# Performance work log

Hardware: AMD Instinct MI355X
Metric: run time of the kernel (lower is better)

Reference implementation:

```python
import jax, jax.numpy as jnp
import numpy as np

SIM_THRESHOLD = 0.7  # suppression threshold on cosine similarity


def setup_inputs() -> dict:
    key = jax.random.key(0)
    k1, k2 = jax.random.split(key)
    tokens = jax.random.normal(k1, (4, 4096, 256), dtype=jnp.float32)
    scores = jax.random.uniform(k2, (4, 4096), dtype=jnp.float32)
    return {"tokens": tokens, "scores": scores}


def _nms_keep_sorted(sim_sorted):
    """Greedy NMS over tokens already sorted by descending score.

    sim_sorted: [N, N] pairwise cosine similarity in sorted order.
    Returns keep mask [N] (bool) in sorted order.
    """
    N = sim_sorted.shape[0]
    idx = jnp.arange(N)

    def step(suppressed, i):
        keep_i = jnp.logical_not(suppressed[i])
        row = sim_sorted[i]  # similarity of token i to all tokens
        # a kept token suppresses all later (lower-score) similar tokens
        suppressed = suppressed | (keep_i & (row > SIM_THRESHOLD) & (idx > i))
        return suppressed, keep_i

    _, keeps = jax.lax.scan(step, jnp.zeros(N, dtype=bool), idx)
    return keeps


def reference(tokens, scores):
    # tokens: [B, N, D], scores: [B, N]
    t = tokens / (jnp.linalg.norm(tokens, axis=-1, keepdims=True) + 1e-6)
    sim = jnp.einsum('bnd,bmd->bnm', t, t)  # [B, N, N] cosine similarity
    order = jnp.argsort(-scores, axis=-1)   # descending score order

    def per_batch(sim_b, order_b):
        sim_sorted = sim_b[order_b][:, order_b]          # reorder rows+cols
        keeps_sorted = _nms_keep_sorted(sim_sorted)      # [N] bool, sorted order
        keep = jnp.zeros_like(keeps_sorted).at[order_b].set(keeps_sorted)
        return keep

    keep = jax.vmap(per_batch)(sim, order)               # [B, N] bool
    masked_tokens = tokens * keep[..., None].astype(tokens.dtype)
    return masked_tokens, keep
```

## Files before the change

kernel.cpp:

```cpp
#include <hip/hip_runtime.h>

#define BATCH 4
#define N 4096
#define D 256
#define THR 0.7f
#define CAP 2048

typedef __attribute__((ext_vector_type(16))) float f32x16;

__device__ __forceinline__ unsigned int fflip(float f) {
    unsigned int u = __float_as_uint(f);
    return (u & 0x80000000u) ? ~u : (u | 0x80000000u);
}

__device__ __forceinline__ void gl_lds16(const unsigned char* g, unsigned char* l) {
    __builtin_amdgcn_global_load_lds(
        (const __attribute__((address_space(1))) unsigned int*)g,
        (__attribute__((address_space(3))) unsigned int*)l, 16, 0, 0);
}

__global__ __launch_bounds__(256) void norm_kernel(const float* __restrict__ tokens,
                                                   unsigned char* __restrict__ ts,
                                                   float* __restrict__ out,
                                                   float* __restrict__ keep_out,
                                                   int* __restrict__ cnt) {
    if (blockIdx.x == 0 && threadIdx.x < BATCH) cnt[threadIdx.x] = 0;
    int gw = (int)((blockIdx.x * 256 + threadIdx.x) >> 6);
    int lane = threadIdx.x & 63;
    const float4* p = (const float4*)(tokens + (size_t)gw * D);
    float4 v = p[lane];
    ((float4*)(out + (size_t)gw * D))[lane] = v;
    if (lane == 0) keep_out[gw] = 1.0f;
    float ss = v.x * v.x + v.y * v.y + v.z * v.z + v.w * v.w;
#pragma unroll
    for (int off = 32; off > 0; off >>= 1) ss += __shfl_xor(ss, off);
    float inv = 1.0f / (sqrtf(ss) + 1e-6f);
    unsigned int u = 0;
    u = __builtin_amdgcn_cvt_pk_fp8_f32(v.x * inv, v.y * inv, u, 0);
    u = __builtin_amdgcn_cvt_pk_fp8_f32(v.z * inv, v.w * inv, u, 1);
    *((unsigned int*)(ts + (size_t)gw * D + lane * 4)) = u;
}

__global__ __launch_bounds__(256, 5) void sim_kernel(const unsigned char* __restrict__ ts,
                                                     const float* __restrict__ scores,
                                                     unsigned long long* __restrict__ edges,
                                                     int* __restrict__ cnt) {
    __shared__ alignas(16) unsigned char smem[32768];
    int p = blockIdx.x;
    int b = blockIdx.y;
    int ti = (int)(32.5f - sqrtf(32.5f * 32.5f - 2.0f * (float)p));
    while (32 * ti - ti * (ti - 1) / 2 > p) --ti;
    while (32 * (ti + 1) - (ti + 1) * ti / 2 <= p) ++ti;
    int tj = ti + (p - (32 * ti - ti * (ti - 1) / 2));

    int t = threadIdx.x;
    int w = t >> 6;
    int L = t & 63;
    const unsigned char* base = ts + (size_t)b * N * D;

    int rl = L >> 3, sl = L & 7;
    const unsigned char* pa = base + (size_t)(ti * 128 + w * 8 + rl) * D + ((sl ^ rl) << 4);
    const unsigned char* pb = base + (size_t)(tj * 128 + w * 8 + rl) * D + ((sl ^ rl) << 4);
    unsigned char* la = smem + w * 1024;
    unsigned char* lb = smem + 16384 + w * 1024;

    int wr = w >> 1, wc = w & 1;
    int m = L & 31, h = L >> 5;
    int aA = (wr * 64 + m) * 128;
    int bB = 16384 + (wc * 64 + m) * 128;
    int swz = m & 7;
    int h8 = h * 8;

    f32x16 acc[2][2] = {};

#pragma unroll
    for (int s = 0; s < 2; ++s) {
#pragma unroll
        for (int i = 0; i < 4; ++i) {
            gl_lds16(pa + (size_t)i * 32 * D, la + i * 4096);
            gl_lds16(pb + (size_t)i * 32 * D, lb + i * 4096);
        }
        pa += 128; pb += 128;
        __syncthreads();
#pragma unroll
        for (int c = 0; c < 8; ++c) {
            int off = ((c ^ swz) << 4) + h8;
            long long a0 = *(const long long*)(smem + aA + off);
            long long a1 = *(const long long*)(smem + aA + 4096 + off);
            long long b0 = *(const long long*)(smem + bB + off);
            long long b1 = *(const long long*)(smem + bB + 4096 + off);
            acc[0][0] = __builtin_amdgcn_mfma_f32_32x32x16_fp8_fp8(a0, b0, acc[0][0], 0, 0, 0);
            acc[0][1] = __builtin_amdgcn_mfma_f32_32x32x16_fp8_fp8(a0, b1, acc[0][1], 0, 0, 0);
            acc[1][0] = __builtin_amdgcn_mfma_f32_32x32x16_fp8_fp8(a1, b0, acc[1][0], 0, 0, 0);
            acc[1][1] = __builtin_amdgcn_mfma_f32_32x32x16_fp8_fp8(a1, b1, acc[1][1], 0, 0, 0);
        }
        __syncthreads();
    }

    {
        float mx = -1e30f;
#pragma unroll
        for (int fa = 0; fa < 2; ++fa)
#pragma unroll
            for (int fb = 0; fb < 2; ++fb)
#pragma unroll
                for (int reg = 0; reg < 16; ++reg)
                    mx = fmaxf(mx, acc[fa][fb][reg]);
        if (!__any(mx > THR)) return;
    }

#pragma unroll
    for (int fa = 0; fa < 2; ++fa) {
#pragma unroll
        for (int fb = 0; fb < 2; ++fb) {
#pragma unroll
            for (int reg = 0; reg < 16; ++reg) {
                int row = (reg & 3) + 8 * (reg >> 2) + 4 * h;
                int ig = ti * 128 + wr * 64 + fa * 32 + row;
                int jg = tj * 128 + wc * 64 + fb * 32 + m;
                float v = acc[fa][fb][reg];
                if (jg > ig && v > THR) {
                    float si = scores[b * N + ig];
                    float sj = scores[b * N + jg];
                    int src, dst;
                    float ssrc;
                    if (si >= sj) { src = ig; dst = jg; ssrc = si; }
                    else          { src = jg; dst = ig; ssrc = sj; }
                    int pos = atomicAdd(&cnt[b], 1);
                    if (pos < CAP) {
                        unsigned long long kk =
                            ((unsigned long long)fflip(ssrc) << 24) |
                            ((unsigned long long)(unsigned int)(4095 - src) << 12) |
                            (unsigned long long)(unsigned int)dst;
                        edges[b * CAP + pos] = kk;
                    }
                }
            }
        }
    }
}

__global__ __launch_bounds__(256) void nms_kernel(const unsigned long long* __restrict__ edges,
                                                  const int* __restrict__ cnt,
                                                  float* __restrict__ keep_out,
                                                  float* __restrict__ out) {
    int b = blockIdx.x;
    __shared__ unsigned long long e[CAP];
    __shared__ unsigned int sup[N / 32];
    int n = cnt[b];
    if (n > CAP) n = CAP;
    if (n > 0) {
        for (int i = threadIdx.x; i < N / 32; i += 256) sup[i] = 0u;
        for (int i = threadIdx.x; i < CAP; i += 256)
            e[i] = (i < n) ? edges[b * CAP + i] : 0ull;
        __syncthreads();
        for (int k = 2; k <= CAP; k <<= 1) {
            for (int j = k >> 1; j > 0; j >>= 1) {
                for (int i = threadIdx.x; i < CAP; i += 256) {
                    int ixj = i ^ j;
                    if (ixj > i) {
                        unsigned long long a = e[i], cc = e[ixj];
                        bool up = ((i & k) == 0);
                        if (up ? (a < cc) : (a > cc)) { e[i] = cc; e[ixj] = a; }
                    }
                }
                __syncthreads();
            }
        }
        if (threadIdx.x == 0) {
            for (int tt = 0; tt < n; ++tt) {
                unsigned long long u = e[tt];
                int src = 4095 - (int)((u >> 12) & 0xFFFu);
                int dst = (int)(u & 0xFFFu);
                if (!((sup[src >> 5] >> (src & 31)) & 1u))
                    sup[dst >> 5] |= 1u << (dst & 31);
            }
        }
        __syncthreads();
        float4 z = make_float4(0.f, 0.f, 0.f, 0.f);
        for (int i = threadIdx.x; i < N; i += 256) {
            if ((sup[i >> 5] >> (i & 31)) & 1u) {
                keep_out[b * N + i] = 0.0f;
                float4* rowp = (float4*)(out + ((size_t)b * N + i) * D);
#pragma unroll
                for (int d = 0; d < D / 4; ++d) rowp[d] = z;
            }
        }
    }
}

extern "C" void kernel_launch(void* const* d_in, const int* in_sizes, int n_in,
                              void* d_out, int out_size, void* d_ws, size_t ws_size,
                              hipStream_t stream) {
    const float* tokens = (const float*)d_in[0];
    const float* scores = (const float*)d_in[1];

    char* ws = (char*)d_ws;
    int* cnt = (int*)ws;
    unsigned long long* edges = (unsigned long long*)(ws + 128);
    unsigned char* ts = (unsigned char*)(ws + 128 + BATCH * CAP * 8);

    float* out = (float*)d_out;
    float* keep_out = out + (size_t)BATCH * N * D;

    norm_kernel<<<(BATCH * N) / 4, 256, 0, stream>>>(tokens, ts, out, keep_out, cnt);
    dim3 g(528, BATCH);
    sim_kernel<<<g, 256, 0, stream>>>(ts, scores, edges, cnt);
    nms_kernel<<<BATCH, 256, 0, stream>>>(edges, cnt, keep_out, out);
}
```

Measured before the change: 91.92 us.

## Double-buffer sim kernel K loop in 64-byte chunks to overlap loads with MFMA

The sim kernel's K dimension is split into four 64-byte stages instead of two 128-byte stages. Two LDS buffers let the global-to-LDS loads for the next stage be issued before the MFMAs on the current stage. The LDS row stride and XOR swizzle are changed to match the 64-byte rows. The aim is to hide global-load latency behind compute, at the cost of more barriers and more loop iterations for a K dimension that is already short.

```diff
diff --git a/kernel.cpp b/kernel.cpp
--- a/kernel.cpp
+++ b/kernel.cpp
@@ -58,37 +58,47 @@
     int L = t & 63;
     const unsigned char* base = ts + (size_t)b * N * D;
 
-    int rl = L >> 3, sl = L & 7;
-    const unsigned char* pa = base + (size_t)(ti * 128 + w * 8 + rl) * D + ((sl ^ rl) << 4);
-    const unsigned char* pb = base + (size_t)(tj * 128 + w * 8 + rl) * D + ((sl ^ rl) << 4);
-    unsigned char* la = smem + w * 1024;
-    unsigned char* lb = smem + 16384 + w * 1024;
+    int rq = L >> 2;
+    int chunk = (L & 3) ^ ((L >> 3) & 3);
+    const unsigned char* pa = base + (size_t)(ti * 128 + w * 32 + rq) * D + (chunk << 4);
+    const unsigned char* pb = base + (size_t)(tj * 128 + w * 32 + rq) * D + (chunk << 4);
+    unsigned int lA = w * 2048u;
+    unsigned int lB = 8192u + w * 2048u;
 
     int wr = w >> 1, wc = w & 1;
     int m = L & 31, h = L >> 5;
-    int aA = (wr * 64 + m) * 128;
-    int bB = 16384 + (wc * 64 + m) * 128;
-    int swz = m & 7;
+    int swz = (m >> 1) & 3;
     int h8 = h * 8;
+    unsigned int aBase = (unsigned int)(wr * 64 + m) * 64u;
+    unsigned int bBase = 8192u + (unsigned int)(wc * 64 + m) * 64u;
 
     f32x16 acc[2][2] = {};
 
-#pragma unroll
-    for (int s = 0; s < 2; ++s) {
-#pragma unroll
-        for (int i = 0; i < 4; ++i) {
-            gl_lds16(pa + (size_t)i * 32 * D, la + i * 4096);
-            gl_lds16(pb + (size_t)i * 32 * D, lb + i * 4096);
-        }
-        pa += 128; pb += 128;
-        __syncthreads();
-#pragma unroll
-        for (int c = 0; c < 8; ++c) {
+    gl_lds16(pa, smem + lA);
+    gl_lds16(pa + 4096, smem + lA + 1024);
+    gl_lds16(pb, smem + lB);
+    gl_lds16(pb + 4096, smem + lB + 1024);
+    __syncthreads();
+
+#pragma unroll
+    for (int ks = 0; ks < 4; ++ks) {
+        unsigned int cur = (unsigned int)(ks & 1) * 16384u;
+        if (ks < 3) {
+            unsigned int nxt = (unsigned int)((ks + 1) & 1) * 16384u;
+            const unsigned char* qa = pa + (ks + 1) * 64;
+            const unsigned char* qb = pb + (ks + 1) * 64;
+            gl_lds16(qa, smem + nxt + lA);
+            gl_lds16(qa + 4096, smem + nxt + lA + 1024);
+            gl_lds16(qb, smem + nxt + lB);
+            gl_lds16(qb + 4096, smem + nxt + lB + 1024);
+        }
+#pragma unroll
+        for (int c = 0; c < 4; ++c) {
             int off = ((c ^ swz) << 4) + h8;
-            long long a0 = *(const long long*)(smem + aA + off);
-            long long a1 = *(const long long*)(smem + aA + 4096 + off);
-            long long b0 = *(const long long*)(smem + bB + off);
-            long long b1 = *(const long long*)(smem + bB + 4096 + off);
+            long long a0 = *(const long long*)(smem + cur + aBase + off);
+            long long a1 = *(const long long*)(smem + cur + aBase + 2048 + off);
+            long long b0 = *(const long long*)(smem + cur + bBase + off);
+            long long b1 = *(const long long*)(smem + cur + bBase + 2048 + off);
             acc[0][0] = __builtin_amdgcn_mfma_f32_32x32x16_fp8_fp8(a0, b0, acc[0][0], 0, 0, 0);
             acc[0][1] = __builtin_amdgcn_mfma_f32_32x32x16_fp8_fp8(a0, b1, acc[0][1], 0, 0, 0);
             acc[1][0] = __builtin_amdgcn_mfma_f32_32x32x16_fp8_fp8(a1, b0, acc[1][0], 0, 0, 0);
```

Result: no change. 90.17 us (-1.9%).
